# Kernel optimization log

Hardware: AMD Instinct MI355X
Metric: run time of the kernel (lower is better)

The kernel has to match this reference:

```python
import jax, jax.numpy as jnp
import numpy as np

N_NODES = 100000
IN_CH = 256
H1, C1 = 8, 8   # conv1: heads=8, out_channels=8
H2, C2 = 1, 3   # conv2: heads=1, out_channels=3
NEG_SLOPE = 0.2
EPS = 1e-16


def gat_conv(x, src, dst, W, a_src, a_dst, b, heads, out_ch, n_nodes):
    """PyG-style GATConv (eval mode, self-loops already in src/dst)."""
    h = (x @ W).reshape(n_nodes, heads, out_ch)          # [N,H,C]
    alpha_s = jnp.einsum('nhc,hc->nh', h, a_src)         # [N,H]
    alpha_d = jnp.einsum('nhc,hc->nh', h, a_dst)         # [N,H]
    e = alpha_s[src] + alpha_d[dst]                      # [E,H]
    e = jnp.where(e > 0, e, NEG_SLOPE * e)               # leaky_relu(0.2)
    # segment softmax over destination nodes
    m = jax.ops.segment_max(e, dst, num_segments=n_nodes)
    m = jnp.where(jnp.isfinite(m), m, 0.0)
    ex = jnp.exp(e - m[dst])
    s = jax.ops.segment_sum(ex, dst, num_segments=n_nodes)
    a = ex / (s[dst] + EPS)                              # [E,H]
    msg = h[src] * a[:, :, None]                         # [E,H,C]
    out = jax.ops.segment_sum(msg, dst, num_segments=n_nodes)  # [N,H,C]
    return out.reshape(n_nodes, heads * out_ch) + b


def setup_inputs() -> dict:
    key = jax.random.key(0)
    ks = jax.random.split(key, 10)
    x = jax.random.normal(ks[0], (N_NODES, IN_CH), dtype=jnp.float32)
    edge_index = jax.random.randint(ks[1], (2, 3200000), 0, N_NODES, dtype=jnp.int64)
    sc = 0.1
    return {
        'x': x,
        'edge_index': edge_index,
        'W1': jax.random.normal(ks[2], (IN_CH, H1 * C1), dtype=jnp.float32) * sc,
        'a_src1': jax.random.normal(ks[3], (H1, C1), dtype=jnp.float32) * sc,
        'a_dst1': jax.random.normal(ks[4], (H1, C1), dtype=jnp.float32) * sc,
        'b1': jnp.zeros((H1 * C1,), dtype=jnp.float32),
        'W2': jax.random.normal(ks[5], (H1 * C1, H2 * C2), dtype=jnp.float32) * sc,
        'a_src2': jax.random.normal(ks[6], (H2, C2), dtype=jnp.float32) * sc,
        'a_dst2': jax.random.normal(ks[7], (H2, C2), dtype=jnp.float32) * sc,
        'b2': jnp.zeros((H2 * C2,), dtype=jnp.float32),
    }


def reference(x, edge_index, W1, a_src1, a_dst1, b1, W2, a_src2, a_dst2, b2):
    n = x.shape[0]
    loop = jnp.arange(n, dtype=edge_index.dtype)
    src = jnp.concatenate([edge_index[0], loop])  # add_self_loops=True
    dst = jnp.concatenate([edge_index[1], loop])
    h = gat_conv(x, src, dst, W1, a_src1, a_dst1, b1, H1, C1, n)
    h = jax.nn.elu(h)
    out = gat_conv(h, src, dst, W2, a_src2, a_dst2, b2, H2, C2, n)
    return out
```

## Files before the change

kernel.cpp:

```cpp
#include <hip/hip_runtime.h>
#include <hip/hip_bf16.h>

#define P_W1  0
#define P_AS1 16384
#define P_AD1 16448
#define P_B1  16512
#define P_W2  16576
#define P_AS2 16768
#define P_AD2 16771
#define P_B2  16774

#define NBLK_CSR 512

typedef __attribute__((ext_vector_type(8))) short short8;
typedef __attribute__((ext_vector_type(8))) unsigned short ushort8v;
typedef __attribute__((ext_vector_type(4))) float floatx4;

__device__ __forceinline__ float ldf(const void* p, int i, int bf) {
  if (bf) {
    unsigned v = ((unsigned)((const unsigned short*)p)[i]) << 16;
    float f; __builtin_memcpy(&f, &v, 4); return f;
  }
  return ((const float*)p)[i];
}
__device__ __forceinline__ int ldi(const void* p, long i, int i64) {
  return i64 ? ((const int*)p)[2*i] : ((const int*)p)[i];
}
__device__ __forceinline__ unsigned short f2bfbits(float f) {
  __hip_bfloat16 b = __float2bfloat16(f);
  unsigned short u; __builtin_memcpy(&u, &b, 2); return u;
}
__device__ __forceinline__ float bf2f(unsigned short u) {
  unsigned v = ((unsigned)u) << 16;
  float f; __builtin_memcpy(&f, &v, 4); return f;
}

__global__ void k_prep(const void* x, const void* ei,
                       const void* w1, const void* as1, const void* ad1, const void* b1,
                       const void* w2, const void* as2, const void* ad2, const void* b2,
                       int* flags, float* params, unsigned short* w1t) {
  __shared__ int sh[2];
  int tid = threadIdx.x, lane = tid & 63, w = tid >> 6;
  if (w == 0) {
    const unsigned* xw = (const unsigned*)x;
    int hits = 0;
    for (int i = lane; i < 256; i += 64) {
      unsigned b = (xw[i] >> 7) & 0xFF;
      hits += (b >= 96 && b <= 141) ? 1 : 0;
    }
    for (int o = 32; o >= 1; o >>= 1) hits += __shfl_xor(hits, o);
    if (lane == 0) sh[0] = (hits >= 160) ? 1 : 0;
  } else if (w == 1) {
    const unsigned* ew = (const unsigned*)ei;
    int z = 0;
    for (int i = lane; i < 128; i += 64) z += (ew[2*i+1] == 0u) ? 1 : 0;
    for (int o = 32; o >= 1; o >>= 1) z += __shfl_xor(z, o);
    if (lane == 0) sh[1] = (z >= 64) ? 1 : 0;
  }
  __syncthreads();
  int bf = sh[0];
  if (tid == 0) { flags[0] = sh[0]; flags[1] = sh[1]; }
  for (int i = tid; i < 16384; i += blockDim.x) {
    int ch = i >> 8, k = i & 255;
    w1t[i] = f2bfbits(ldf(w1, k * 64 + ch, bf));
  }
  if (!bf) {
    for (int i = tid; i < 16384; i += blockDim.x) params[P_W1 + i] = ldf(w1, i, bf);
  }
  for (int i = tid; i < 64; i += blockDim.x) {
    params[P_AS1 + i] = ldf(as1, i, bf);
    params[P_AD1 + i] = ldf(ad1, i, bf);
    params[P_B1  + i] = ldf(b1,  i, bf);
  }
  for (int i = tid; i < 192; i += blockDim.x) params[P_W2 + i] = ldf(w2, i, bf);
  for (int i = tid; i < 3; i += blockDim.x) {
    params[P_AS2 + i] = ldf(as2, i, bf);
    params[P_AD2 + i] = ldf(ad2, i, bf);
    params[P_B2  + i] = ldf(b2,  i, bf);
  }
}

__global__ void k_bcount(const void* ei, const int* flags, int* gcnt, int* brsv,
                         int E0, int N, int NB, int chunk) {
  __shared__ int h[256];
  int tid = threadIdx.x;
  int i64 = flags[1];
  for (int j = tid; j < NB; j += 256) h[j] = 0;
  __syncthreads();
  int E = E0 + N;
  int b0 = blockIdx.x * chunk, b1 = min(b0 + chunk, E);
  for (int e = b0 + tid; e < b1; e += 256) {
    int dst = (e < E0) ? ldi(ei, (long)E0 + e, i64) : (e - E0);
    atomicAdd(&h[dst >> 9], 1);
  }
  __syncthreads();
  for (int j = tid; j < NB; j += 256)
    brsv[blockIdx.x * NB + j] = atomicAdd(&gcnt[j], h[j]);
}

__global__ void k_bbase(const int* gcnt, int* bbase, int NB) {
  __shared__ int sh[256];
  int tid = threadIdx.x;
  sh[tid] = (tid < NB) ? gcnt[tid] : 0;
  __syncthreads();
  int own = sh[tid];
  for (int ofs = 1; ofs < 256; ofs <<= 1) {
    int v = (tid >= ofs) ? sh[tid - ofs] : 0;
    __syncthreads();
    sh[tid] += v;
    __syncthreads();
  }
  if (tid < NB) bbase[tid] = sh[tid] - own;
  if (tid == NB - 1) bbase[NB] = sh[tid];
}

__global__ void k_bscatter(const void* ei, const int* flags, const int* bbase,
                           const int* brsv, unsigned* pairs, int E0, int N, int NB, int chunk) {
  __shared__ int base_s[256];
  __shared__ int rnk[256];
  int i64 = flags[1], tid = threadIdx.x;
  for (int j = tid; j < NB; j += 256) {
    base_s[j] = bbase[j] + brsv[blockIdx.x * NB + j];
    rnk[j] = 0;
  }
  __syncthreads();
  int E = E0 + N;
  int b0 = blockIdx.x * chunk, b1 = min(b0 + chunk, E);
  for (int e = b0 + tid; e < b1; e += 256) {
    int src, dst;
    if (e < E0) { src = ldi(ei, e, i64); dst = ldi(ei, (long)E0 + e, i64); }
    else        { src = e - E0; dst = src; }
    int bkt = dst >> 9;
    int r = atomicAdd(&rnk[bkt], 1);
    pairs[base_s[bkt] + r] = ((unsigned)src << 9) | (unsigned)(dst & 511);
  }
}

__device__ __forceinline__ void gemm1_f32(const float* x, const float* params,
                                          unsigned short* h1, float* a_s, float* a_d,
                                          int N, int wave, int lane) {
  int n0 = wave * 4;
  if (n0 >= N) return;
  int nb[4];
#pragma unroll
  for (int j = 0; j < 4; j++) nb[j] = min(n0 + j, N - 1) * 256;
  float acc[4] = {0.f, 0.f, 0.f, 0.f};
  const float* W = params + P_W1;
  for (int k = 0; k < 256; k++) {
    float wv = W[k * 64 + lane];
#pragma unroll
    for (int j = 0; j < 4; j++) acc[j] += x[nb[j] + k] * wv;
  }
  float as1v = params[P_AS1 + lane], ad1v = params[P_AD1 + lane];
#pragma unroll
  for (int j = 0; j < 4; j++) {
    int n = n0 + j;
    if (n >= N) break;
    float hv = acc[j];
    float s = hv * as1v, d = hv * ad1v;
    s += __shfl_xor(s, 1); s += __shfl_xor(s, 2); s += __shfl_xor(s, 4);
    d += __shfl_xor(d, 1); d += __shfl_xor(d, 2); d += __shfl_xor(d, 4);
    h1[(size_t)n * 64 + lane] = f2bfbits(hv);
    if ((lane & 7) == 0) {
      a_s[n * 8 + (lane >> 3)] = s;
      a_d[n * 8 + (lane >> 3)] = d;
    }
  }
}

__global__ void k_bsort_gemm1(const unsigned* pairs, const int* bbase, int* rowp, int* srcs,
                              const void* x, const unsigned short* w1t, const int* flags,
                              const float* params, unsigned short* h1, float* a_s, float* a_d,
                              int N, int NB, int E) {
  __shared__ __align__(16) char smem[32768];
  int tid = threadIdx.x;
  if ((int)blockIdx.x < NB) {
    int* h0 = (int*)smem;
    int* sc = h0 + 512;
    int* rk = sc + 512;
    int b = blockIdx.x;
    int s0 = bbase[b], s1 = bbase[b + 1], L = s1 - s0;
    for (int j = tid; j < 512; j += 256) { h0[j] = 0; rk[j] = 0; }
    __syncthreads();
    for (int i = tid; i < L; i += 256) atomicAdd(&h0[pairs[s0 + i] & 511], 1);
    __syncthreads();
    for (int j = tid; j < 512; j += 256) sc[j] = h0[j];
    __syncthreads();
    for (int ofs = 1; ofs < 512; ofs <<= 1) {
      int j0 = tid, j1 = tid + 256;
      int v0 = (j0 >= ofs) ? sc[j0 - ofs] : 0;
      int v1 = (j1 >= ofs) ? sc[j1 - ofs] : 0;
      __syncthreads();
      sc[j0] += v0; sc[j1] += v1;
      __syncthreads();
    }
    for (int j = tid; j < 512; j += 256) {
      int off = sc[j] - h0[j];
      int node = (b << 9) + j;
      if (node < N) rowp[node] = s0 + off;
      sc[j] = off;
    }
    if (b == 0 && tid == 0) rowp[N] = E;
    __syncthreads();
    for (int i = tid; i < L; i += 256) {
      unsigned p = pairs[s0 + i];
      int j = p & 511;
      int r = atomicAdd(&rk[j], 1);
      srcs[s0 + sc[j] + r] = (int)(p >> 9);
    }
    return;
  }
  int tile = blockIdx.x - NB;
  int w = tid >> 6, lane = tid & 63;
  if (flags[0]) {
    int row0 = tile << 6;
    int l16 = lane & 15, quad = lane >> 4;
    int ch = w * 16 + l16;
    const char* xb = (const char*)x;
#pragma unroll
    for (int j = 0; j < 8; j++) {
      int g = w * 512 + j * 64 + lane;
      int r = g >> 5;
      int p = (g & 31) << 4;
      int gr = row0 + r; if (gr >= N) gr = N - 1;
      const char* src = xb + (size_t)gr * 512 + (size_t)(p ^ ((r & 7) << 4));
      char* dst = smem + w * 8192 + j * 1024 + lane * 16;
      __builtin_amdgcn_global_load_lds((const __attribute__((address_space(1))) unsigned int*)src,
                                       (__attribute__((address_space(3))) unsigned int*)dst,
                                       16, 0, 0);
    }
    short8 bfr[8];
    const unsigned short* wp = w1t + (size_t)ch * 256 + quad * 8;
#pragma unroll
    for (int i = 0; i < 8; i++) bfr[i] = *(const short8*)(wp + i * 32);
    __syncthreads();
    floatx4 acc[4];
#pragma unroll
    for (int rg = 0; rg < 4; rg++) {
      floatx4 a4 = {0.f, 0.f, 0.f, 0.f};
      int r = rg * 16 + l16;
      const char* arow = smem + r * 512;
      int swz = (r & 7) << 4;
#pragma unroll
      for (int i = 0; i < 8; i++) {
        short8 afr = *(const short8*)(arow + ((quad * 16 + i * 64) ^ swz));
        a4 = __builtin_amdgcn_mfma_f32_16x16x32_bf16(afr, bfr[i], a4, 0, 0, 0);
      }
      acc[rg] = a4;
    }
    __syncthreads();
    float* ht = (float*)smem;
#pragma unroll
    for (int rg = 0; rg < 4; rg++)
#pragma unroll
      for (int rr = 0; rr < 4; rr++)
        ht[(rg * 16 + quad * 4 + rr) * 68 + ch] = acc[rg][rr];
    __syncthreads();
    int t = tid;
#pragma unroll
    for (int it = 0; it < 2; it++, t += 256) {
      int nl = t >> 3, head = t & 7;
      int n = row0 + nl;
      if (n < N) {
        const float* hr = ht + nl * 68 + head * 8;
        float s = 0.f, d = 0.f;
        ushort8v u;
#pragma unroll
        for (int c = 0; c < 8; c++) {
          float v = hr[c];
          s += v * params[P_AS1 + head * 8 + c];
          d += v * params[P_AD1 + head * 8 + c];
          u[c] = f2bfbits(v);
        }
        *(ushort8v*)(h1 + (size_t)n * 64 + head * 8) = u;
        a_s[n * 8 + head] = s;
        a_d[n * 8 + head] = d;
      }
    }
  } else {
    for (int k4 = 0; k4 < 4; k4++)
      gemm1_f32((const float*)x, params, h1, a_s, a_d, N, tile * 16 + w * 4 + k4, lane);
  }
}

__global__ void k_agg1(const float* params, const unsigned short* h1, const float* a_s,
                       const float* a_d, const int* rowp, const int* srcs,
                       float4* pk, float* ad2, int N) {
  int n = blockIdx.x * (blockDim.x >> 6) + (threadIdx.x >> 6);
  int lane = threadIdx.x & 63;
  if (n >= N) return;
  int start = rowp[n], end = rowp[n + 1];
  int h = lane & 7, es = lane >> 3;
  float adh = a_d[n * 8 + h];
  float m = -1e30f;
  for (int i = start + es; i < end; i += 8) {
    float e = a_s[srcs[i] * 8 + h] + adh;
    e = e > 0.f ? e : 0.2f * e;
    m = fmaxf(m, e);
  }
  m = fmaxf(m, __shfl_xor(m, 8));
  m = fmaxf(m, __shfl_xor(m, 16));
  m = fmaxf(m, __shfl_xor(m, 32));
  float acc[8] = {0.f,0.f,0.f,0.f,0.f,0.f,0.f,0.f};
  float ssum = 0.f;
  for (int i = start + es; i < end; i += 8) {
    int s = srcs[i];
    float e = a_s[s * 8 + h] + adh;
    e = e > 0.f ? e : 0.2f * e;
    float ex = __expf(e - m);
    ssum += ex;
    ushort8v u = *(const ushort8v*)(h1 + (size_t)s * 64 + h * 8);
#pragma unroll
    for (int c = 0; c < 8; c++) acc[c] += ex * bf2f(u[c]);
  }
#pragma unroll
  for (int msk = 8; msk <= 32; msk <<= 1) {
    ssum += __shfl_xor(ssum, msk);
#pragma unroll
    for (int c = 0; c < 8; c++) acc[c] += __shfl_xor(acc[c], msk);
  }
  if (es == 0) {
    float inv = 1.f / (ssum + 1e-16f);
    float pj0 = 0.f, pj1 = 0.f, pj2 = 0.f;
#pragma unroll
    for (int c = 0; c < 8; c++) {
      float v = acc[c] * inv + params[P_B1 + h * 8 + c];
      v = v > 0.f ? v : (__expf(v) - 1.f);
      const float* w2r = params + P_W2 + (h * 8 + c) * 3;
      pj0 += v * w2r[0]; pj1 += v * w2r[1]; pj2 += v * w2r[2];
    }
    pj0 += __shfl_xor(pj0, 1); pj1 += __shfl_xor(pj1, 1); pj2 += __shfl_xor(pj2, 1);
    pj0 += __shfl_xor(pj0, 2); pj1 += __shfl_xor(pj1, 2); pj2 += __shfl_xor(pj2, 2);
    pj0 += __shfl_xor(pj0, 4); pj1 += __shfl_xor(pj1, 4); pj2 += __shfl_xor(pj2, 4);
    if (h == 0) {
      float as2 = pj0*params[P_AS2+0] + pj1*params[P_AS2+1] + pj2*params[P_AS2+2];
      float ad2v = pj0*params[P_AD2+0] + pj1*params[P_AD2+1] + pj2*params[P_AD2+2];
      pk[n] = make_float4(pj0, pj1, pj2, as2);
      ad2[n] = ad2v;
    }
  }
}

__global__ void k_agg2(const float* params, const float4* pk, const float* ad2,
                       const int* rowp, const int* srcs, void* out, const int* flags, int N) {
  int wid = blockIdx.x * (blockDim.x >> 6) + (threadIdx.x >> 6);
  int lane = threadIdx.x & 63;
  int g = lane >> 4, t = lane & 15;
  int n = wid * 4 + g;
  if (n >= N) return;
  int start = rowp[n], end = rowp[n + 1];
  float ad = ad2[n];
  float m = -1e30f;
  for (int i = start + t; i < end; i += 16) {
    float e = pk[srcs[i]].w + ad;
    e = e > 0.f ? e : 0.2f * e;
    m = fmaxf(m, e);
  }
#pragma unroll
  for (int msk = 1; msk <= 8; msk <<= 1) m = fmaxf(m, __shfl_xor(m, msk));
  float ssum = 0.f, c0 = 0.f, c1 = 0.f, c2 = 0.f;
  for (int i = start + t; i < end; i += 16) {
    float4 v = pk[srcs[i]];
    float e = v.w + ad;
    e = e > 0.f ? e : 0.2f * e;
    float ex = __expf(e - m);
    ssum += ex;
    c0 += ex * v.x; c1 += ex * v.y; c2 += ex * v.z;
  }
#pragma unroll
  for (int msk = 1; msk <= 8; msk <<= 1) {
    ssum += __shfl_xor(ssum, msk);
    c0 += __shfl_xor(c0, msk); c1 += __shfl_xor(c1, msk); c2 += __shfl_xor(c2, msk);
  }
  if (t == 0) {
    float inv = 1.f / (ssum + 1e-16f);
    float o0 = c0 * inv + params[P_B2+0];
    float o1 = c1 * inv + params[P_B2+1];
    float o2 = c2 * inv + params[P_B2+2];
    if (flags[0]) {
      __hip_bfloat16* ob = (__hip_bfloat16*)out;
      ob[n*3+0] = __float2bfloat16(o0);
      ob[n*3+1] = __float2bfloat16(o1);
      ob[n*3+2] = __float2bfloat16(o2);
    } else {
      float* of = (float*)out;
      of[n*3+0] = o0; of[n*3+1] = o1; of[n*3+2] = o2;
    }
  }
}

extern "C" void kernel_launch(void* const* d_in, const int* in_sizes, int n_in,
                              void* d_out, int out_size, void* d_ws, size_t ws_size,
                              hipStream_t stream) {
  const void* x  = d_in[0];
  const void* ei = d_in[1];
  int N  = in_sizes[0] / 256;
  int E0 = in_sizes[1] / 2;
  int E  = E0 + N;
  int NB = (N + 511) >> 9;
  int chunk = (E + NBLK_CSR - 1) / NBLK_CSR;
  int ntile = (N + 63) >> 6;

  char* w = (char*)d_ws;
  size_t off = 0;
  auto alloc = [&](size_t bytes) -> char* {
    char* p = w + off;
    off += (bytes + 255) & ~(size_t)255;
    return p;
  };
  int*            flags  = (int*)           alloc(256);
  float*          params = (float*)         alloc(17408 * 4);
  unsigned short* w1t    = (unsigned short*)alloc(16384 * 2);
  unsigned short* h1     = (unsigned short*)alloc((size_t)N * 64 * 2);
  float*          a_s1   = (float*)         alloc((size_t)N * 8 * 4);
  float*          a_d1   = (float*)         alloc((size_t)N * 8 * 4);
  float4*         pk     = (float4*)        alloc((size_t)N * 16);
  float*          ad2    = (float*)         alloc((size_t)N * 4);
  int*            gcnt   = (int*)           alloc(256 * 4);
  int*            bbase  = (int*)           alloc(257 * 4);
  int*            brsv   = (int*)           alloc((size_t)NBLK_CSR * NB * 4);
  int*            rowp   = (int*)           alloc((size_t)(N + 1) * 4);
  unsigned*       pairs  = (unsigned*)      alloc((size_t)E * 4);
  int*            srcs   = (int*)           alloc((size_t)E * 4);
  (void)ws_size; (void)n_in; (void)out_size;

  hipMemsetAsync(gcnt, 0, 256 * 4, stream);
  k_prep<<<1, 256, 0, stream>>>(x, ei, d_in[2], d_in[3], d_in[4], d_in[5],
                                d_in[6], d_in[7], d_in[8], d_in[9], flags, params, w1t);
  k_bcount<<<dim3(NBLK_CSR), 256, 0, stream>>>(ei, flags, gcnt, brsv, E0, N, NB, chunk);
  k_bbase<<<1, 256, 0, stream>>>(gcnt, bbase, NB);
  k_bscatter<<<dim3(NBLK_CSR), 256, 0, stream>>>(ei, flags, bbase, brsv, pairs, E0, N, NB, chunk);
  k_bsort_gemm1<<<dim3(NB + ntile), 256, 0, stream>>>(pairs, bbase, rowp, srcs, x, w1t, flags,
                                                      params, h1, a_s1, a_d1, N, NB, E);
  k_agg1<<<dim3((N + 3) / 4), 256, 0, stream>>>(params, h1, a_s1, a_d1, rowp, srcs, pk, ad2, N);
  k_agg2<<<dim3((N + 15) / 16), 256, 0, stream>>>(params, pk, ad2, rowp, srcs, d_out, flags, N);
}
```

Before: 704.9 us.

## Replace two-level bucket sort CSR build with global atomic histogram and scatter

Builds the CSR with a per-node global atomic histogram, a two-pass block scan, and an atomic-cursor scatter of sources. This replaces the previous bucketed count, scatter, and per-bucket local sort that was fused with the first GEMM. The GEMM now runs as its own kernel with 32-row tiles to get more blocks. Global atomics on 100k counters and non-deterministic edge order within rows trade against removing the pairs buffer and the extra bucket-sort pass.

After: 1.013 ms. 43.7% more time.

```diff
diff --git a/kernel.cpp b/kernel.cpp
--- a/kernel.cpp
+++ b/kernel.cpp
@@ -10,7 +10,7 @@
 #define P_AD2 16771
 #define P_B2  16774
 
-#define NBLK_CSR 512
+#define NBLK_E 512
 
 typedef __attribute__((ext_vector_type(8))) short short8;
 typedef __attribute__((ext_vector_type(8))) unsigned short ushort8v;
@@ -80,59 +80,71 @@
   }
 }
 
-__global__ void k_bcount(const void* ei, const int* flags, int* gcnt, int* brsv,
-                         int E0, int N, int NB, int chunk) {
-  __shared__ int h[256];
-  int tid = threadIdx.x;
-  int i64 = flags[1];
-  for (int j = tid; j < NB; j += 256) h[j] = 0;
+__global__ void k_hist(const void* ei, const int* flags, int* rowcnt, int E0, int chunk) {
+  int i64 = flags[1], tid = threadIdx.x;
+  int b0 = blockIdx.x * chunk, b1 = min(b0 + chunk, E0);
+  for (int e = b0 + tid; e < b1; e += 256) {
+    int dst = ldi(ei, (long)E0 + e, i64);
+    atomicAdd(&rowcnt[dst], 1);
+  }
+}
+
+__global__ void k_scan1(const int* rowcnt, int* rowp, int* bsum, int N) {
+  __shared__ int sh[256];
+  int b = blockIdx.x, tid = threadIdx.x;
+  int base = b * 1024 + tid * 4;
+  int v0 = 0, v1 = 0, v2 = 0, v3 = 0;
+  if (base + 0 < N) v0 = rowcnt[base + 0] + 1;
+  if (base + 1 < N) v1 = rowcnt[base + 1] + 1;
+  if (base + 2 < N) v2 = rowcnt[base + 2] + 1;
+  if (base + 3 < N) v3 = rowcnt[base + 3] + 1;
+  int t = v0 + v1 + v2 + v3;
+  sh[tid] = t;
   __syncthreads();
-  int E = E0 + N;
-  int b0 = blockIdx.x * chunk, b1 = min(b0 + chunk, E);
-  for (int e = b0 + tid; e < b1; e += 256) {
-    int dst = (e < E0) ? ldi(ei, (long)E0 + e, i64) : (e - E0);
-    atomicAdd(&h[dst >> 9], 1);
+  for (int ofs = 1; ofs < 256; ofs <<= 1) {
+    int u = (tid >= ofs) ? sh[tid - ofs] : 0;
+    __syncthreads();
+    sh[tid] += u;
+    __syncthreads();
+  }
+  int p = sh[tid] - t;
+  if (tid == 255) bsum[b] = sh[255];
+  if (base + 0 < N) rowp[base + 0] = p; p += v0;
+  if (base + 1 < N) rowp[base + 1] = p; p += v1;
+  if (base + 2 < N) rowp[base + 2] = p; p += v2;
+  if (base + 3 < N) rowp[base + 3] = p;
+}
+
+__global__ void k_scan2(const int* bsum, int* rowp, int* cursor, int N, int NBK, int E) {
+  __shared__ int off_s;
+  int b = blockIdx.x, tid = threadIdx.x;
+  if (tid == 0) {
+    int o = 0;
+    for (int j = 0; j < b; j++) o += bsum[j];
+    off_s = o;
   }
   __syncthreads();
-  for (int j = tid; j < NB; j += 256)
-    brsv[blockIdx.x * NB + j] = atomicAdd(&gcnt[j], h[j]);
-}
-
-__global__ void k_bbase(const int* gcnt, int* bbase, int NB) {
-  __shared__ int sh[256];
-  int tid = threadIdx.x;
-  sh[tid] = (tid < NB) ? gcnt[tid] : 0;
-  __syncthreads();
-  int own = sh[tid];
-  for (int ofs = 1; ofs < 256; ofs <<= 1) {
-    int v = (tid >= ofs) ? sh[tid - ofs] : 0;
-    __syncthreads();
-    sh[tid] += v;
-    __syncthreads();
-  }
-  if (tid < NB) bbase[tid] = sh[tid] - own;
-  if (tid == NB - 1) bbase[NB] = sh[tid];
-}
-
-__global__ void k_bscatter(const void* ei, const int* flags, const int* bbase,
-                           const int* brsv, unsigned* pairs, int E0, int N, int NB, int chunk) {
-  __shared__ int base_s[256];
-  __shared__ int rnk[256];
+  int off = off_s;
+  int base = b * 1024 + tid * 4;
+#pragma unroll
+  for (int j = 0; j < 4; j++) {
+    int n = base + j;
+    if (n < N) { int r = rowp[n] + off; rowp[n] = r; cursor[n] = r; }
+  }
+  if (b == NBK - 1 && tid == 0) rowp[N] = E;
+}
+
+__global__ void k_scatter(const void* ei, const int* flags, int* cursor, int* srcs,
+                          int E0, int N, int chunk) {
   int i64 = flags[1], tid = threadIdx.x;
-  for (int j = tid; j < NB; j += 256) {
-    base_s[j] = bbase[j] + brsv[blockIdx.x * NB + j];
-    rnk[j] = 0;
-  }
-  __syncthreads();
   int E = E0 + N;
   int b0 = blockIdx.x * chunk, b1 = min(b0 + chunk, E);
   for (int e = b0 + tid; e < b1; e += 256) {
     int src, dst;
     if (e < E0) { src = ldi(ei, e, i64); dst = ldi(ei, (long)E0 + e, i64); }
     else        { src = e - E0; dst = src; }
-    int bkt = dst >> 9;
-    int r = atomicAdd(&rnk[bkt], 1);
-    pairs[base_s[bkt] + r] = ((unsigned)src << 9) | (unsigned)(dst & 511);
+    int pos = atomicAdd(&cursor[dst], 1);
+    srcs[pos] = src;
   }
 }
 
@@ -168,63 +180,25 @@
   }
 }
 
-__global__ void k_bsort_gemm1(const unsigned* pairs, const int* bbase, int* rowp, int* srcs,
-                              const void* x, const unsigned short* w1t, const int* flags,
-                              const float* params, unsigned short* h1, float* a_s, float* a_d,
-                              int N, int NB, int E) {
-  __shared__ __align__(16) char smem[32768];
+__global__ void k_gemm1(const void* x, const unsigned short* w1t, const int* flags,
+                        const float* params, unsigned short* h1, float* a_s, float* a_d, int N) {
+  __shared__ __align__(16) char smem[16384];
   int tid = threadIdx.x;
-  if ((int)blockIdx.x < NB) {
-    int* h0 = (int*)smem;
-    int* sc = h0 + 512;
-    int* rk = sc + 512;
-    int b = blockIdx.x;
-    int s0 = bbase[b], s1 = bbase[b + 1], L = s1 - s0;
-    for (int j = tid; j < 512; j += 256) { h0[j] = 0; rk[j] = 0; }
-    __syncthreads();
-    for (int i = tid; i < L; i += 256) atomicAdd(&h0[pairs[s0 + i] & 511], 1);
-    __syncthreads();
-    for (int j = tid; j < 512; j += 256) sc[j] = h0[j];
-    __syncthreads();
-    for (int ofs = 1; ofs < 512; ofs <<= 1) {
-      int j0 = tid, j1 = tid + 256;
-      int v0 = (j0 >= ofs) ? sc[j0 - ofs] : 0;
-      int v1 = (j1 >= ofs) ? sc[j1 - ofs] : 0;
-      __syncthreads();
-      sc[j0] += v0; sc[j1] += v1;
-      __syncthreads();
-    }
-    for (int j = tid; j < 512; j += 256) {
-      int off = sc[j] - h0[j];
-      int node = (b << 9) + j;
-      if (node < N) rowp[node] = s0 + off;
-      sc[j] = off;
-    }
-    if (b == 0 && tid == 0) rowp[N] = E;
-    __syncthreads();
-    for (int i = tid; i < L; i += 256) {
-      unsigned p = pairs[s0 + i];
-      int j = p & 511;
-      int r = atomicAdd(&rk[j], 1);
-      srcs[s0 + sc[j] + r] = (int)(p >> 9);
-    }
-    return;
-  }
-  int tile = blockIdx.x - NB;
+  int tile = blockIdx.x;
   int w = tid >> 6, lane = tid & 63;
   if (flags[0]) {
-    int row0 = tile << 6;
+    int row0 = tile << 5;
     int l16 = lane & 15, quad = lane >> 4;
     int ch = w * 16 + l16;
     const char* xb = (const char*)x;
 #pragma unroll
-    for (int j = 0; j < 8; j++) {
-      int g = w * 512 + j * 64 + lane;
-      int r = g >> 5;
-      int p = (g & 31) << 4;
+    for (int j = 0; j < 4; j++) {
+      int g = w * 256 + j * 64 + lane;
+      int r = g >> 4;
+      int p = (g & 15) << 4;
       int gr = row0 + r; if (gr >= N) gr = N - 1;
       const char* src = xb + (size_t)gr * 512 + (size_t)(p ^ ((r & 7) << 4));
-      char* dst = smem + w * 8192 + j * 1024 + lane * 16;
+      char* dst = smem + w * 4096 + j * 1024 + lane * 16;
       __builtin_amdgcn_global_load_lds((const __attribute__((address_space(1))) unsigned int*)src,
                                        (__attribute__((address_space(3))) unsigned int*)dst,
                                        16, 0, 0);
@@ -234,9 +208,9 @@
 #pragma unroll
     for (int i = 0; i < 8; i++) bfr[i] = *(const short8*)(wp + i * 32);
     __syncthreads();
-    floatx4 acc[4];
-#pragma unroll
-    for (int rg = 0; rg < 4; rg++) {
+    floatx4 acc[2];
+#pragma unroll
+    for (int rg = 0; rg < 2; rg++) {
       floatx4 a4 = {0.f, 0.f, 0.f, 0.f};
       int r = rg * 16 + l16;
       const char* arow = smem + r * 512;
@@ -251,35 +225,31 @@
     __syncthreads();
     float* ht = (float*)smem;
 #pragma unroll
-    for (int rg = 0; rg < 4; rg++)
+    for (int rg = 0; rg < 2; rg++)
 #pragma unroll
       for (int rr = 0; rr < 4; rr++)
         ht[(rg * 16 + quad * 4 + rr) * 68 + ch] = acc[rg][rr];
     __syncthreads();
-    int t = tid;
-#pragma unroll
-    for (int it = 0; it < 2; it++, t += 256) {
-      int nl = t >> 3, head = t & 7;
-      int n = row0 + nl;
-      if (n < N) {
-        const float* hr = ht + nl * 68 + head * 8;
-        float s = 0.f, d = 0.f;
-        ushort8v u;
-#pragma unroll
-        for (int c = 0; c < 8; c++) {
-          float v = hr[c];
-          s += v * params[P_AS1 + head * 8 + c];
-          d += v * params[P_AD1 + head * 8 + c];
-          u[c] = f2bfbits(v);
-        }
-        *(ushort8v*)(h1 + (size_t)n * 64 + head * 8) = u;
-        a_s[n * 8 + head] = s;
-        a_d[n * 8 + head] = d;
+    int nl = tid >> 3, head = tid & 7;
+    int n = row0 + nl;
+    if (n < N) {
+      const float* hr = ht + nl * 68 + head * 8;
+      float s = 0.f, d = 0.f;
+      ushort8v u;
+#pragma unroll
+      for (int c = 0; c < 8; c++) {
+        float v = hr[c];
+        s += v * params[P_AS1 + head * 8 + c];
+        d += v * params[P_AD1 + head * 8 + c];
+        u[c] = f2bfbits(v);
       }
+      *(ushort8v*)(h1 + (size_t)n * 64 + head * 8) = u;
+      a_s[n * 8 + head] = s;
+      a_d[n * 8 + head] = d;
     }
   } else {
-    for (int k4 = 0; k4 < 4; k4++)
-      gemm1_f32((const float*)x, params, h1, a_s, a_d, N, tile * 16 + w * 4 + k4, lane);
+    for (int k4 = 0; k4 < 2; k4++)
+      gemm1_f32((const float*)x, params, h1, a_s, a_d, N, tile * 8 + w * 2 + k4, lane);
   }
 }
 
@@ -397,9 +367,10 @@
   int N  = in_sizes[0] / 256;
   int E0 = in_sizes[1] / 2;
   int E  = E0 + N;
-  int NB = (N + 511) >> 9;
-  int chunk = (E + NBLK_CSR - 1) / NBLK_CSR;
-  int ntile = (N + 63) >> 6;
+  int NBK = (N + 1023) >> 10;
+  int chunk0 = (E0 + NBLK_E - 1) / NBLK_E;
+  int chunkE = (E  + NBLK_E - 1) / NBLK_E;
+  int ntile = (N + 31) >> 5;
 
   char* w = (char*)d_ws;
   size_t off = 0;
@@ -416,22 +387,21 @@
   float*          a_d1   = (float*)         alloc((size_t)N * 8 * 4);
   float4*         pk     = (float4*)        alloc((size_t)N * 16);
   float*          ad2    = (float*)         alloc((size_t)N * 4);
-  int*            gcnt   = (int*)           alloc(256 * 4);
-  int*            bbase  = (int*)           alloc(257 * 4);
-  int*            brsv   = (int*)           alloc((size_t)NBLK_CSR * NB * 4);
+  int*            rowcnt = (int*)           alloc((size_t)N * 4);
   int*            rowp   = (int*)           alloc((size_t)(N + 1) * 4);
-  unsigned*       pairs  = (unsigned*)      alloc((size_t)E * 4);
+  int*            cursor = (int*)           alloc((size_t)N * 4);
+  int*            bsum   = (int*)           alloc((size_t)NBK * 4);
   int*            srcs   = (int*)           alloc((size_t)E * 4);
   (void)ws_size; (void)n_in; (void)out_size;
 
-  hipMemsetAsync(gcnt, 0, 256 * 4, stream);
+  hipMemsetAsync(rowcnt, 0, (size_t)N * 4, stream);
   k_prep<<<1, 256, 0, stream>>>(x, ei, d_in[2], d_in[3], d_in[4], d_in[5],
                                 d_in[6], d_in[7], d_in[8], d_in[9], flags, params, w1t);
-  k_bcount<<<dim3(NBLK_CSR), 256, 0, stream>>>(ei, flags, gcnt, brsv, E0, N, NB, chunk);
-  k_bbase<<<1, 256, 0, stream>>>(gcnt, bbase, NB);
-  k_bscatter<<<dim3(NBLK_CSR), 256, 0, stream>>>(ei, flags, bbase, brsv, pairs, E0, N, NB, chunk);
-  k_bsort_gemm1<<<dim3(NB + ntile), 256, 0, stream>>>(pairs, bbase, rowp, srcs, x, w1t, flags,
-                                                      params, h1, a_s1, a_d1, N, NB, E);
+  k_gemm1<<<dim3(ntile), 256, 0, stream>>>(x, w1t, flags, params, h1, a_s1, a_d1, N);
+  k_hist<<<dim3(NBLK_E), 256, 0, stream>>>(ei, flags, rowcnt, E0, chunk0);
+  k_scan1<<<dim3(NBK), 256, 0, stream>>>(rowcnt, rowp, bsum, N);
+  k_scan2<<<dim3(NBK), 256, 0, stream>>>(bsum, rowp, cursor, N, NBK, E);
+  k_scatter<<<dim3(NBLK_E), 256, 0, stream>>>(ei, flags, cursor, srcs, E0, N, chunkE);
   k_agg1<<<dim3((N + 3) / 4), 256, 0, stream>>>(params, h1, a_s1, a_d1, rowp, srcs, pk, ad2, N);
   k_agg2<<<dim3((N + 15) / 16), 256, 0, stream>>>(params, pk, ad2, rowp, srcs, d_out, flags, N);
 }
```

## Split bucket sort from GEMM1 and make GEMM1 a persistent double-buffered kernel

Applied to the files above, without the earlier changes.

The fused bucket-sort plus GEMM1 kernel becomes two kernels. GEMM1 now runs as a persistent grid of 1024 blocks over 32-row tiles and double-buffers its global-to-LDS loads, so the next tile's fetch overlaps the current tile's MFMA work. It also launches right after prep, ahead of the CSR build kernels, and the LDS row stride changes from 68 to 67. The aim is to hide x-load latency and get rid of the imbalance of mixing sort blocks with GEMM tiles in one grid, at the cost of one extra launch and smaller tiles.

Result: faster. 682.9 us (-3.1%).

```diff
diff --git a/kernel.cpp b/kernel.cpp
--- a/kernel.cpp
+++ b/kernel.cpp
@@ -11,6 +11,7 @@
 #define P_B2  16774
 
 #define NBLK_CSR 512
+#define G1GRID   1024
 
 typedef __attribute__((ext_vector_type(8))) short short8;
 typedef __attribute__((ext_vector_type(8))) unsigned short ushort8v;
@@ -33,6 +34,13 @@
 __device__ __forceinline__ float bf2f(unsigned short u) {
   unsigned v = ((unsigned)u) << 16;
   float f; __builtin_memcpy(&f, &v, 4); return f;
+}
+
+__device__ __forceinline__ void bar_lgkm() {
+  __builtin_amdgcn_sched_barrier(0);
+  asm volatile("s_waitcnt lgkmcnt(0)" ::: "memory");
+  __builtin_amdgcn_s_barrier();
+  __builtin_amdgcn_sched_barrier(0);
 }
 
 __global__ void k_prep(const void* x, const void* ei,
@@ -136,6 +144,41 @@
   }
 }
 
+__global__ void k_bsort(const unsigned* pairs, const int* bbase, int* rowp,
+                        int* srcs, int N, int NB, int E) {
+  __shared__ int h0[512], sc[512], rk[512];
+  int b = blockIdx.x, tid = threadIdx.x;
+  int s0 = bbase[b], s1 = bbase[b + 1], L = s1 - s0;
+  for (int j = tid; j < 512; j += 256) { h0[j] = 0; rk[j] = 0; }
+  __syncthreads();
+  for (int i = tid; i < L; i += 256) atomicAdd(&h0[pairs[s0 + i] & 511], 1);
+  __syncthreads();
+  for (int j = tid; j < 512; j += 256) sc[j] = h0[j];
+  __syncthreads();
+  for (int ofs = 1; ofs < 512; ofs <<= 1) {
+    int j0 = tid, j1 = tid + 256;
+    int v0 = (j0 >= ofs) ? sc[j0 - ofs] : 0;
+    int v1 = (j1 >= ofs) ? sc[j1 - ofs] : 0;
+    __syncthreads();
+    sc[j0] += v0; sc[j1] += v1;
+    __syncthreads();
+  }
+  for (int j = tid; j < 512; j += 256) {
+    int off = sc[j] - h0[j];
+    int node = (b << 9) + j;
+    if (node < N) rowp[node] = s0 + off;
+    sc[j] = off;
+  }
+  if (b == 0 && tid == 0) rowp[N] = E;
+  __syncthreads();
+  for (int i = tid; i < L; i += 256) {
+    unsigned p = pairs[s0 + i];
+    int j = p & 511;
+    int r = atomicAdd(&rk[j], 1);
+    srcs[s0 + sc[j] + r] = (int)(p >> 9);
+  }
+}
+
 __device__ __forceinline__ void gemm1_f32(const float* x, const float* params,
                                           unsigned short* h1, float* a_s, float* a_d,
                                           int N, int wave, int lane) {
@@ -168,101 +211,74 @@
   }
 }
 
-__global__ void k_bsort_gemm1(const unsigned* pairs, const int* bbase, int* rowp, int* srcs,
-                              const void* x, const unsigned short* w1t, const int* flags,
-                              const float* params, unsigned short* h1, float* a_s, float* a_d,
-                              int N, int NB, int E) {
+__global__ void k_gemm1(const void* x, const unsigned short* w1t, const int* flags,
+                        const float* params, unsigned short* h1, float* a_s, float* a_d, int N) {
   __shared__ __align__(16) char smem[32768];
   int tid = threadIdx.x;
-  if ((int)blockIdx.x < NB) {
-    int* h0 = (int*)smem;
-    int* sc = h0 + 512;
-    int* rk = sc + 512;
-    int b = blockIdx.x;
-    int s0 = bbase[b], s1 = bbase[b + 1], L = s1 - s0;
-    for (int j = tid; j < 512; j += 256) { h0[j] = 0; rk[j] = 0; }
-    __syncthreads();
-    for (int i = tid; i < L; i += 256) atomicAdd(&h0[pairs[s0 + i] & 511], 1);
-    __syncthreads();
-    for (int j = tid; j < 512; j += 256) sc[j] = h0[j];
-    __syncthreads();
-    for (int ofs = 1; ofs < 512; ofs <<= 1) {
-      int j0 = tid, j1 = tid + 256;
-      int v0 = (j0 >= ofs) ? sc[j0 - ofs] : 0;
-      int v1 = (j1 >= ofs) ? sc[j1 - ofs] : 0;
-      __syncthreads();
-      sc[j0] += v0; sc[j1] += v1;
-      __syncthreads();
-    }
-    for (int j = tid; j < 512; j += 256) {
-      int off = sc[j] - h0[j];
-      int node = (b << 9) + j;
-      if (node < N) rowp[node] = s0 + off;
-      sc[j] = off;
-    }
-    if (b == 0 && tid == 0) rowp[N] = E;
-    __syncthreads();
-    for (int i = tid; i < L; i += 256) {
-      unsigned p = pairs[s0 + i];
-      int j = p & 511;
-      int r = atomicAdd(&rk[j], 1);
-      srcs[s0 + sc[j] + r] = (int)(p >> 9);
-    }
-    return;
-  }
-  int tile = blockIdx.x - NB;
   int w = tid >> 6, lane = tid & 63;
   if (flags[0]) {
-    int row0 = tile << 6;
+    int NT = (N + 31) >> 5;
     int l16 = lane & 15, quad = lane >> 4;
     int ch = w * 16 + l16;
     const char* xb = (const char*)x;
-#pragma unroll
-    for (int j = 0; j < 8; j++) {
-      int g = w * 512 + j * 64 + lane;
-      int r = g >> 5;
-      int p = (g & 31) << 4;
-      int gr = row0 + r; if (gr >= N) gr = N - 1;
-      const char* src = xb + (size_t)gr * 512 + (size_t)(p ^ ((r & 7) << 4));
-      char* dst = smem + w * 8192 + j * 1024 + lane * 16;
-      __builtin_amdgcn_global_load_lds((const __attribute__((address_space(1))) unsigned int*)src,
-                                       (__attribute__((address_space(3))) unsigned int*)dst,
-                                       16, 0, 0);
-    }
+
+    auto stage = [&](int t, int bsel) {
+      int row0 = t << 5;
+      char* buf = smem + bsel * 16384;
+#pragma unroll
+      for (int jj = 0; jj < 4; jj++) {
+        int g = w * 256 + jj * 64 + lane;
+        int r = g >> 5;
+        int c = g & 31;
+        int gr = row0 + r; if (gr >= N) gr = N - 1;
+        const char* src = xb + (size_t)gr * 512 + (size_t)((c << 4) ^ ((r & 7) << 4));
+        char* dst = buf + g * 16;
+        __builtin_amdgcn_global_load_lds((const __attribute__((address_space(1))) unsigned int*)src,
+                                         (__attribute__((address_space(3))) unsigned int*)dst,
+                                         16, 0, 0);
+      }
+    };
+
     short8 bfr[8];
     const unsigned short* wp = w1t + (size_t)ch * 256 + quad * 8;
 #pragma unroll
     for (int i = 0; i < 8; i++) bfr[i] = *(const short8*)(wp + i * 32);
-    __syncthreads();
-    floatx4 acc[4];
-#pragma unroll
-    for (int rg = 0; rg < 4; rg++) {
-      floatx4 a4 = {0.f, 0.f, 0.f, 0.f};
-      int r = rg * 16 + l16;
-      const char* arow = smem + r * 512;
-      int swz = (r & 7) << 4;
-#pragma unroll
-      for (int i = 0; i < 8; i++) {
-        short8 afr = *(const short8*)(arow + ((quad * 16 + i * 64) ^ swz));
-        a4 = __builtin_amdgcn_mfma_f32_16x16x32_bf16(afr, bfr[i], a4, 0, 0, 0);
+    __builtin_amdgcn_sched_barrier(0);
+
+    int t0 = blockIdx.x;
+    if (t0 < NT) stage(t0, 0);
+    int cur = 0;
+    for (int t = t0; t < NT; t += G1GRID) {
+      __syncthreads();
+      if (t + G1GRID < NT) stage(t + G1GRID, cur ^ 1);
+      int row0 = t << 5;
+      const char* buf = smem + cur * 16384;
+      floatx4 acc[2];
+#pragma unroll
+      for (int rg = 0; rg < 2; rg++) {
+        floatx4 a4 = {0.f, 0.f, 0.f, 0.f};
+        int r = rg * 16 + l16;
+        const char* arow = buf + r * 512;
+        int swz = (r & 7) << 4;
+#pragma unroll
+        for (int i = 0; i < 8; i++) {
+          short8 afr = *(const short8*)(arow + ((quad * 16 + i * 64) ^ swz));
+          a4 = __builtin_amdgcn_mfma_f32_16x16x32_bf16(afr, bfr[i], a4, 0, 0, 0);
+        }
+        acc[rg] = a4;
       }
-      acc[rg] = a4;
-    }
-    __syncthreads();
-    float* ht = (float*)smem;
-#pragma unroll
-    for (int rg = 0; rg < 4; rg++)
-#pragma unroll
-      for (int rr = 0; rr < 4; rr++)
-        ht[(rg * 16 + quad * 4 + rr) * 68 + ch] = acc[rg][rr];
-    __syncthreads();
-    int t = tid;
-#pragma unroll
-    for (int it = 0; it < 2; it++, t += 256) {
-      int nl = t >> 3, head = t & 7;
+      bar_lgkm();
+      float* ht = (float*)(smem + cur * 16384);
+#pragma unroll
+      for (int rg = 0; rg < 2; rg++)
+#pragma unroll
+        for (int rr = 0; rr < 4; rr++)
+          ht[(rg * 16 + quad * 4 + rr) * 67 + ch] = acc[rg][rr];
+      bar_lgkm();
+      int nl = tid >> 3, head = tid & 7;
       int n = row0 + nl;
       if (n < N) {
-        const float* hr = ht + nl * 68 + head * 8;
+        const float* hr = ht + nl * 67 + head * 8;
         float s = 0.f, d = 0.f;
         ushort8v u;
 #pragma unroll
@@ -276,10 +292,12 @@
         a_s[n * 8 + head] = s;
         a_d[n * 8 + head] = d;
       }
+      cur ^= 1;
     }
   } else {
-    for (int k4 = 0; k4 < 4; k4++)
-      gemm1_f32((const float*)x, params, h1, a_s, a_d, N, tile * 16 + w * 4 + k4, lane);
+    int NW = (N + 3) >> 2;
+    for (int task = blockIdx.x * 4 + w; task < NW; task += G1GRID * 4)
+      gemm1_f32((const float*)x, params, h1, a_s, a_d, N, task, lane);
   }
 }
 
@@ -399,7 +417,6 @@
   int E  = E0 + N;
   int NB = (N + 511) >> 9;
   int chunk = (E + NBLK_CSR - 1) / NBLK_CSR;
-  int ntile = (N + 63) >> 6;
 
   char* w = (char*)d_ws;
   size_t off = 0;
@@ -427,11 +444,11 @@
   hipMemsetAsync(gcnt, 0, 256 * 4, stream);
   k_prep<<<1, 256, 0, stream>>>(x, ei, d_in[2], d_in[3], d_in[4], d_in[5],
                                 d_in[6], d_in[7], d_in[8], d_in[9], flags, params, w1t);
+  k_gemm1<<<dim3(G1GRID), 256, 0, stream>>>(x, w1t, flags, params, h1, a_s1, a_d1, N);
   k_bcount<<<dim3(NBLK_CSR), 256, 0, stream>>>(ei, flags, gcnt, brsv, E0, N, NB, chunk);
   k_bbase<<<1, 256, 0, stream>>>(gcnt, bbase, NB);
   k_bscatter<<<dim3(NBLK_CSR), 256, 0, stream>>>(ei, flags, bbase, brsv, pairs, E0, N, NB, chunk);
-  k_bsort_gemm1<<<dim3(NB + ntile), 256, 0, stream>>>(pairs, bbase, rowp, srcs, x, w1t, flags,
-                                                      params, h1, a_s1, a_d1, N, NB, E);
+  k_bsort<<<dim3(NB), 256, 0, stream>>>(pairs, bbase, rowp, srcs, N, NB, E);
   k_agg1<<<dim3((N + 3) / 4), 256, 0, stream>>>(params, h1, a_s1, a_d1, rowp, srcs, pk, ad2, N);
   k_agg2<<<dim3((N + 15) / 16), 256, 0, stream>>>(params, pk, ad2, rowp, srcs, d_out, flags, N);
 }
```
